# Optimization experiments

Hardware: AMD Instinct MI355X
Metric: run time of the kernel (lower is better)

The kernel has to match this reference:

```python
import jax, jax.numpy as jnp
import numpy as np

B, D, L = 8, 512, 4096
NHEAD = 8
HEAD_DIM = D // NHEAD
TRUNC_STD = 0.02


def setup_inputs() -> dict:
    key = jax.random.key(0)
    ks = jax.random.split(key, 7)
    return {
        "x": jax.random.normal(ks[0], (B, D, L, 1), jnp.float32),
        "y": jax.random.normal(ks[1], (B, D, 1, 1), jnp.float32),
        "Wq": jax.random.normal(ks[2], (D, D), jnp.float32) * TRUNC_STD,
        "Wk": jax.random.normal(ks[3], (D, D), jnp.float32) * TRUNC_STD,
        "Wv": jax.random.normal(ks[4], (D, D), jnp.float32) * TRUNC_STD,
        "WO_ring": jax.random.normal(ks[5], (D, D), jnp.float32) * TRUNC_STD,
        "bO_ring": jnp.zeros((D,), jnp.float32),
        "WO_star": jax.random.normal(ks[6], (D, D), jnp.float32) * TRUNC_STD,
        "bO_star": jnp.zeros((D,), jnp.float32),
    }


def reference(x, y, Wq, Wk, Wv, WO_ring, bO_ring, WO_star, bO_star):
    Bx, Dx, Lx, _ = x.shape
    hd = Dx // NHEAD
    scale = 1.0 / np.sqrt(hd).astype(np.float32)

    # concat relay token on the sequence axis, project q/k/v over channels
    xy = jnp.concatenate([x, y], axis=2)[..., 0]            # [B, D, L+1]
    xy = jnp.transpose(xy, (0, 2, 1))                       # [B, L+1, D]
    q = jnp.transpose(xy @ Wq, (0, 2, 1))                   # [B, D, L+1]
    k = jnp.transpose(xy @ Wk, (0, 2, 1))
    v = jnp.transpose(xy @ Wv, (0, 2, 1))

    # ---- ring (local window-3 + relay) attention over the L node tokens ----
    qn = q[:, :, :Lx].reshape(Bx, NHEAD, hd, Lx)            # [B,n,h,L]
    kn, vn = k[:, :, :Lx], v[:, :, :Lx]                     # [B,D,L]
    kr, vr = k[:, :, Lx], v[:, :, Lx]                       # [B,D]

    def window3(t):
        # extract_patches SAME with size 3: slot w holds t[:, :, l-1+w], zero-padded
        tp = jnp.pad(t, ((0, 0), (0, 0), (1, 1)))
        tw = jnp.stack([tp[:, :, w:w + Lx] for w in range(3)], axis=2)  # [B,D,3,L]
        return tw.reshape(Bx, NHEAD, hd, 3, Lx)

    kr_b = jnp.broadcast_to(kr.reshape(Bx, NHEAD, hd, 1, 1), (Bx, NHEAD, hd, 1, Lx))
    vr_b = jnp.broadcast_to(vr.reshape(Bx, NHEAD, hd, 1, 1), (Bx, NHEAD, hd, 1, Lx))
    kw = jnp.concatenate([window3(kn), kr_b], axis=3)       # [B,n,h,4,L]
    vw = jnp.concatenate([window3(vn), vr_b], axis=3)

    scores = jnp.einsum('bnhl,bnhwl->bnwl', qn, kw) * scale  # [B,n,4,L]
    alphas = jax.nn.softmax(scores, axis=2)                  # softmax over window
    att = jnp.einsum('bnwl,bnhwl->bnhl', alphas, vw).reshape(Bx, Dx, Lx)
    nodes = jnp.einsum('bdl,de->bel', att, WO_ring) + bO_ring[None, :, None]
    nodes = nodes[..., None]                                 # [B, D, L, 1]

    # ---- star (relay) attention: relay query attends to all L+1 tokens ----
    qr = q[:, :, Lx].reshape(Bx, NHEAD, 1, hd)              # [B,n,1,h]
    ka = k.reshape(Bx, NHEAD, hd, Lx + 1)                   # [B,n,h,L+1]
    va = v.reshape(Bx, NHEAD, hd, Lx + 1)
    s = jnp.einsum('bnoh,bnhl->bnol', qr, ka) * scale       # [B,n,1,L+1]
    a = jax.nn.softmax(s, axis=-1)
    att_r = jnp.einsum('bnol,bnhl->bnoh', a, va).reshape(Bx, Dx)
    relay = (att_r @ WO_star + bO_star).reshape(Bx, Dx, 1, 1)

    return nodes, relay
```

## Files before the change

kernel.cpp:

```cpp
#include <hip/hip_runtime.h>

#define BB 8
#define DD 512
#define LL 4096
#define NH 8
#define HD 64
#define SCALE 0.125f
#define NCH 16
#define CH 256

typedef __attribute__((ext_vector_type(8))) short short8;
typedef __attribute__((ext_vector_type(4))) float f32x4;

static __device__ __forceinline__ float bf2f(unsigned short u) {
  union { float f; unsigned int i; } c; c.i = ((unsigned int)u) << 16; return c.f;
}
static __device__ __forceinline__ unsigned short f2bf(float f) {
  union { float f; unsigned int i; } c; c.f = f;
  unsigned int i = c.i;
  unsigned int r = (i + 0x7fffu + ((i >> 16) & 1u)) >> 16;
  return (unsigned short)r;
}

static __device__ __forceinline__ void gload_lds16(const void* g, void* l) {
  __builtin_amdgcn_global_load_lds(
      (const __attribute__((address_space(1))) void*)g,
      (__attribute__((address_space(3))) void*)l, 16, 0, 0);
}

static __device__ __forceinline__ float waveSum(float v) {
#pragma unroll
  for (int o = 32; o; o >>= 1) v += __shfl_down(v, o, 64);
  return v;
}
static __device__ __forceinline__ float waveMax(float v) {
#pragma unroll
  for (int o = 32; o; o >>= 1) v = fmaxf(v, __shfl_down(v, o, 64));
  return v;
}
static __device__ __forceinline__ float grp8Sum(float v) {
  v += __shfl_xor(v, 1, 8);
  v += __shfl_xor(v, 2, 8);
  v += __shfl_xor(v, 4, 8);
  return v;
}
static __device__ float blockSum(float v, float* red) {
  const int lane = threadIdx.x & 63, wid = threadIdx.x >> 6;
  const int nw = (int)(blockDim.x >> 6);
  v = waveSum(v);
  if (lane == 0) red[wid] = v;
  __syncthreads();
  if (wid == 0) {
    float t = (lane < nw) ? red[lane] : 0.f;
    t = waveSum(t);
    if (lane == 0) red[0] = t;
  }
  __syncthreads();
  float r = red[0];
  __syncthreads();
  return r;
}
static __device__ float blockMax(float v, float* red) {
  const int lane = threadIdx.x & 63, wid = threadIdx.x >> 6;
  const int nw = (int)(blockDim.x >> 6);
  v = waveMax(v);
  if (lane == 0) red[wid] = v;
  __syncthreads();
  if (wid == 0) {
    float t = (lane < nw) ? red[lane] : -1e30f;
    t = waveMax(t);
    if (lane == 0) red[0] = t;
  }
  __syncthreads();
  float r = red[0];
  __syncthreads();
  return r;
}

__global__ __launch_bounds__(256) void prep_w4(
    const float* __restrict__ w0, const float* __restrict__ w1,
    const float* __restrict__ w2, const float* __restrict__ w3,
    unsigned short* __restrict__ o0, unsigned short* __restrict__ o1,
    unsigned short* __restrict__ o2, unsigned short* __restrict__ o3) {
  const int s = blockIdx.z;
  const float* win = (s == 0) ? w0 : (s == 1) ? w1 : (s == 2) ? w2 : w3;
  unsigned short* wout = (s == 0) ? o0 : (s == 1) ? o1 : (s == 2) ? o2 : o3;
  const int d0 = blockIdx.y * 64;
  const int m0 = blockIdx.x * 64;
  __shared__ float t[64][65];
  const int tid = threadIdx.x;
  const int r = tid >> 4;
  const int c4 = (tid & 15) * 4;
#pragma unroll
  for (int p = 0; p < 4; p++) {
    const float4 v = *(const float4*)(win + (size_t)(d0 + p * 16 + r) * DD + m0 + c4);
    *(float4*)&t[p * 16 + r][c4] = v;
  }
  __syncthreads();
#pragma unroll
  for (int p = 0; p < 4; p++) {
    const int ll = p * 16 + r;
    ushort4 o;
    o.x = f2bf(t[c4 + 0][ll]);
    o.y = f2bf(t[c4 + 1][ll]);
    o.z = f2bf(t[c4 + 2][ll]);
    o.w = f2bf(t[c4 + 3][ll]);
    *(ushort4*)(wout + (size_t)(m0 + ll) * DD + d0 + c4) = o;
  }
}

__global__ __launch_bounds__(256) void prep_x(
    const float* __restrict__ x, unsigned short* __restrict__ xt) {
  const int b = blockIdx.z;
  const int e0 = blockIdx.y * 64;
  const int l0 = blockIdx.x * 64;
  __shared__ float t[64][65];
  const int tid = threadIdx.x;
  const int r = tid >> 4;
  const int c4 = (tid & 15) * 4;
  const float* xb = x + (size_t)b * DD * LL;
#pragma unroll
  for (int p = 0; p < 4; p++) {
    const float4 v = *(const float4*)(xb + (size_t)(e0 + p * 16 + r) * LL + l0 + c4);
    *(float4*)&t[p * 16 + r][c4] = v;
  }
  __syncthreads();
#pragma unroll
  for (int p = 0; p < 4; p++) {
    const int ll = p * 16 + r;
    ushort4 o;
    o.x = f2bf(t[c4 + 0][ll]);
    o.y = f2bf(t[c4 + 1][ll]);
    o.z = f2bf(t[c4 + 2][ll]);
    o.w = f2bf(t[c4 + 3][ll]);
    *(ushort4*)(xt + ((size_t)b * LL + l0 + ll) * DD + e0 + c4) = o;
  }
}

#define STAGEH(g, s)                                       \
  do {                                                     \
    gload_lds16((g) + sgoff, (s) + sloff);                 \
    gload_lds16((g) + sgoff + 32, (s) + sloff + 4096);     \
  } while (0)

#define READ_A(dst, base, ib)                                           \
  _Pragma("unroll") for (int i = 0; i < 4; i++) {                       \
    dst[i][0] = *(const short8*)((base) + ((ib) + i) * 512);            \
    dst[i][1] = *(const short8*)((base) + ((ib) + i) * 512 + 4096);     \
  }

#define READ_B(base, qn_)                                               \
  _Pragma("unroll") for (int j = 0; j < 2; j++) {                       \
    bb[j][0] = *(const short8*)((base) + (qn_) * 1024 + j * 512);       \
    bb[j][1] = *(const short8*)((base) + (qn_) * 1024 + j * 512 + 4096);\
  }

#define MFMA16(AF, IO, JO)                                                    \
  __builtin_amdgcn_s_setprio(1);                                              \
  _Pragma("unroll") for (int i = 0; i < 4; i++)                               \
  _Pragma("unroll") for (int j = 0; j < 2; j++) {                             \
    acc[(IO) + i][(JO) + j] = __builtin_amdgcn_mfma_f32_16x16x32_bf16(        \
        AF[i][0], bb[j][0], acc[(IO) + i][(JO) + j], 0, 0, 0);                \
    acc[(IO) + i][(JO) + j] = __builtin_amdgcn_mfma_f32_16x16x32_bf16(        \
        AF[i][1], bb[j][1], acc[(IO) + i][(JO) + j], 0, 0, 0);                \
  }                                                                           \
  __builtin_amdgcn_s_setprio(0);

#define PHASE_SYNC_PRE                                     \
  __builtin_amdgcn_s_barrier();                            \
  asm volatile("s_waitcnt lgkmcnt(0)" ::: "memory");       \
  __builtin_amdgcn_sched_barrier(0);

#define PHASE_SYNC_POST                                    \
  __builtin_amdgcn_sched_barrier(0);                       \
  __builtin_amdgcn_s_barrier();

__global__ __launch_bounds__(512, 2) void qkv_mfma_8ph(
    const unsigned short* __restrict__ Wt, const unsigned short* __restrict__ Xt,
    unsigned short* __restrict__ qn, unsigned short* __restrict__ kn,
    unsigned short* __restrict__ vn) {
  extern __shared__ __align__(16) unsigned short sm[];
  const int wgid = blockIdx.x + 16 * (blockIdx.y + 6 * blockIdx.z);
  const int swz = (wgid & 7) * 96 + (wgid >> 3);
  const int b = swz / 96;
  const int rem = swz - b * 96;
  const int n0 = (rem / 6) * 256;
  const int m0 = (rem % 6) * 256;
  const int tid = threadIdx.x;
  const int lane = tid & 63, w = tid >> 6;
  const int wm = w >> 2, wn = w & 3;
  const int l15 = lane & 15, lh = lane >> 4;

  const unsigned short* Ag = Wt + (size_t)m0 * DD;
  const unsigned short* Bg = Xt + ((size_t)b * LL + n0) * DD;

  const int kswz = (lh << 3) ^ ((l15 & 8) << 1);
  const unsigned short* aB = sm + wm * 8192 + l15 * 32 + kswz;
  const unsigned short* bB = sm + 32768 + (wn >> 1) * 8192 + (wn & 1) * 2048 +
                             l15 * 32 + kswz;

  const int srow = (w << 4) + (lane >> 2);
  const size_t sgoff = (size_t)srow * DD + ((size_t)(((lane & 3) << 3) ^ ((srow & 8) << 1)));
  const int sloff = w * 512;

  f32x4 acc[8][4];
#pragma unroll
  for (int i = 0; i < 8; i++)
#pragma unroll
    for (int j = 0; j < 4; j++) acc[i][j] = (f32x4){0.f, 0.f, 0.f, 0.f};

  STAGEH(Ag, sm);
  STAGEH(Ag + 128 * DD, sm + 8192);
  STAGEH(Bg, sm + 32768);
  STAGEH(Bg + 128 * DD, sm + 32768 + 8192);
  STAGEH(Ag + 64, sm + 16384);
  STAGEH(Ag + 128 * DD + 64, sm + 16384 + 8192);
  asm volatile("s_waitcnt vmcnt(4)" ::: "memory");
  __builtin_amdgcn_s_barrier();

  short8 a0[4][2], a1[4][2], bb[2][2];
  for (int u = 0; u < 8; ++u) {
    const int slot = u & 1;
    const unsigned short* aS = aB + slot * 16384;
    const unsigned short* bS = bB + slot * 16384;
    const unsigned short* An = Ag + (u + 2) * 64;
    const unsigned short* Bn = Bg + (u + 1) * 64;
    unsigned short* sAd = sm + slot * 16384;
    unsigned short* sBd = sm + 32768 + (slot ^ 1) * 16384;

    READ_A(a0, aS, 0);
    READ_B(bS, 0);
    if (u < 7) STAGEH(Bn, sBd);
    PHASE_SYNC_PRE
    MFMA16(a0, 0, 0)
    PHASE_SYNC_POST
    READ_A(a1, aS, 4);
    if (u < 7) STAGEH(Bn + 128 * DD, sBd + 8192);
    PHASE_SYNC_PRE
    MFMA16(a1, 4, 0)
    PHASE_SYNC_POST
    READ_B(bS, 1);
    if (u < 6) STAGEH(An, sAd);
    PHASE_SYNC_PRE
    MFMA16(a0, 0, 2)
    PHASE_SYNC_POST
    if (u < 6) STAGEH(An + 128 * DD, sAd + 8192);
    __builtin_amdgcn_s_barrier();
    asm volatile("s_waitcnt lgkmcnt(0)" ::: "memory");
    __builtin_amdgcn_sched_barrier(0);
    MFMA16(a1, 4, 2)
    __builtin_amdgcn_sched_barrier(0);
    if (u < 6) {
      asm volatile("s_waitcnt vmcnt(4)" ::: "memory");
    } else if (u == 6) {
      asm volatile("s_waitcnt vmcnt(0)" ::: "memory");
    }
    __builtin_amdgcn_s_barrier();
  }

  __syncthreads();
#pragma unroll
  for (int i = 0; i < 8; i++)
#pragma unroll
    for (int j = 0; j < 4; j++) {
      const int dloc = wm * 128 + i * 16 + lh * 4;
      const int lloc = wn * 64 + j * 16 + l15;
      ushort4 pk;
      pk.x = f2bf(acc[i][j][0]);
      pk.y = f2bf(acc[i][j][1]);
      pk.z = f2bf(acc[i][j][2]);
      pk.w = f2bf(acc[i][j][3]);
      *(ushort4*)((char*)sm + ((lloc * 512 + dloc * 2) ^ ((lloc & 7) << 4))) = pk;
    }
  __syncthreads();
  const int sector = m0 >> 9;
  unsigned short* outp = ((sector == 0) ? qn : (sector == 1) ? kn : vn) +
                         (size_t)b * LL * DD + (m0 & 511);
#pragma unroll
  for (int it = 0; it < 16; it++) {
    const int flat = it * 8192 + tid * 16;
    const int lloc = flat >> 9;
    const int off = flat & 511;
    const short8 vdat =
        *(const short8*)((const char*)sm + lloc * 512 + (off ^ ((lloc & 7) << 4)));
    *(short8*)(outp + (size_t)(n0 + lloc) * DD + (off >> 1)) = vdat;
  }
}

__global__ __launch_bounds__(256) void nodes_mfma(
    const unsigned short* __restrict__ Wt, const unsigned short* __restrict__ At,
    const float* __restrict__ bo, float* __restrict__ out) {
  const int wgid = blockIdx.x + 32 * (blockIdx.y + 4 * blockIdx.z);
  const int swz = (wgid & 7) * 128 + (wgid >> 3);
  const int b = swz >> 7;
  const int rem = swz & 127;
  const int n0 = (rem >> 2) * 128;
  const int m0 = (rem & 3) * 128;
  __shared__ short As[128 * 32];
  __shared__ short Bs[128 * 32];
  const int tid = threadIdx.x;
  const int lane = tid & 63, w = tid >> 6;
  const int wm = w & 1, wn = w >> 1;

  const unsigned short* Ag = Wt + (size_t)m0 * DD;
  const unsigned short* Bg = At + ((size_t)b * LL + n0) * DD;
  const int srow = lane >> 2;
  const int scol = (lane & 3) * 8;

  f32x4 acc[4][4];
#pragma unroll
  for (int i = 0; i < 4; i++)
#pragma unroll
    for (int j = 0; j < 4; j++) acc[i][j] = (f32x4){0.f, 0.f, 0.f, 0.f};

  for (int k0 = 0; k0 < DD; k0 += 32) {
    __syncthreads();
#pragma unroll
    for (int p = 0; p < 2; p++) {
      const int c = w * 2 + p;
      gload_lds16(Ag + (size_t)(c * 16 + srow) * DD + k0 + scol, (short*)As + c * 16 * 32);
      gload_lds16(Bg + (size_t)(c * 16 + srow) * DD + k0 + scol, (short*)Bs + c * 16 * 32);
    }
    __syncthreads();
    short8 af[4], bfr[4];
#pragma unroll
    for (int i = 0; i < 4; i++)
      af[i] = *(const short8*)&As[(wm * 64 + i * 16 + (lane & 15)) * 32 + (lane >> 4) * 8];
#pragma unroll
    for (int j = 0; j < 4; j++)
      bfr[j] = *(const short8*)&Bs[(wn * 64 + j * 16 + (lane & 15)) * 32 + (lane >> 4) * 8];
#pragma unroll
    for (int i = 0; i < 4; i++)
#pragma unroll
      for (int j = 0; j < 4; j++)
        acc[i][j] = __builtin_amdgcn_mfma_f32_16x16x32_bf16(af[i], bfr[j], acc[i][j], 0, 0, 0);
  }

  float* outp = out + (size_t)b * DD * LL;
  const int ebase = m0 + wm * 64;
  const int col0 = n0 + wn * 64 + (lane & 15);
#pragma unroll
  for (int i = 0; i < 4; i++) {
    const int e0 = ebase + i * 16 + (lane >> 4) * 4;
#pragma unroll
    for (int j = 0; j < 4; j++) {
      const int cc = col0 + j * 16;
#pragma unroll
      for (int r = 0; r < 4; r++)
        outp[(size_t)(e0 + r) * LL + cc] = acc[i][j][r] + bo[e0 + r];
    }
  }
}

__global__ __launch_bounds__(256) void relay_qkv(
    const float* __restrict__ y, const float* __restrict__ Wq,
    const float* __restrict__ Wk, const float* __restrict__ Wv,
    float* __restrict__ qr, float* __restrict__ kr, float* __restrict__ vr) {
  const int b = blockIdx.y;
  const int d = blockIdx.x * 256 + threadIdx.x;
  __shared__ float ys[DD];
  for (int i = threadIdx.x; i < DD; i += 256) ys[i] = y[b * DD + i];
  __syncthreads();
  float aq = 0.f, ak = 0.f, av = 0.f;
  for (int e = 0; e < DD; e++) {
    const float yv = ys[e];
    aq = fmaf(yv, Wq[(size_t)e * DD + d], aq);
    ak = fmaf(yv, Wk[(size_t)e * DD + d], ak);
    av = fmaf(yv, Wv[(size_t)e * DD + d], av);
  }
  qr[b * DD + d] = aq;
  kr[b * DD + d] = ak;
  vr[b * DD + d] = av;
}

__global__ __launch_bounds__(256) void local_attn(
    const unsigned short* __restrict__ qn, const unsigned short* __restrict__ kn,
    const unsigned short* __restrict__ vn, const float* __restrict__ kr,
    const float* __restrict__ vr, unsigned short* __restrict__ att_t) {
  const int b = blockIdx.z, n = blockIdx.y;
  const int tid = threadIdx.x;
  const int li = tid >> 3, dl = tid & 7;
  const int l = blockIdx.x * 32 + li;
  __shared__ float krs[HD], vrs[HD];
  const int rb = b * DD + n * HD;
  if (tid < HD) { krs[tid] = kr[rb + tid]; vrs[tid] = vr[rb + tid]; }
  __syncthreads();

  const size_t rowbase = ((size_t)b * LL + l) * DD + n * HD + dl * 8;
  const unsigned short* qp = qn + rowbase;
  const unsigned short* kp = kn + rowbase;
  const unsigned short* vp = vn + rowbase;
  const bool has_m = (l > 0), has_p = (l < LL - 1);
  const long moff = has_m ? -(long)DD : 0;
  const long poff = has_p ? (long)DD : 0;

  const short8 q8 = *(const short8*)qp;
  const short8 km8 = *(const short8*)(kp + moff);
  const short8 k08 = *(const short8*)kp;
  const short8 kp8 = *(const short8*)(kp + poff);

  float s0 = 0.f, s1 = 0.f, s2 = 0.f, s3 = 0.f;
  float qf[8];
#pragma unroll
  for (int j = 0; j < 8; j++) {
    qf[j] = bf2f((unsigned short)q8[j]);
    s0 = fmaf(qf[j], bf2f((unsigned short)km8[j]), s0);
    s1 = fmaf(qf[j], bf2f((unsigned short)k08[j]), s1);
    s2 = fmaf(qf[j], bf2f((unsigned short)kp8[j]), s2);
    s3 = fmaf(qf[j], krs[dl * 8 + j], s3);
  }
  s0 = grp8Sum(s0) * SCALE;
  s1 = grp8Sum(s1) * SCALE;
  s2 = grp8Sum(s2) * SCALE;
  s3 = grp8Sum(s3) * SCALE;
  if (!has_m) s0 = 0.f;
  if (!has_p) s2 = 0.f;
  const float m = fmaxf(fmaxf(s0, s1), fmaxf(s2, s3));
  const float e0 = __expf(s0 - m), e1 = __expf(s1 - m);
  const float e2 = __expf(s2 - m), e3 = __expf(s3 - m);
  const float inv = 1.f / (e0 + e1 + e2 + e3);
  const float a0 = has_m ? e0 * inv : 0.f;
  const float a1 = e1 * inv;
  const float a2 = has_p ? e2 * inv : 0.f;
  const float a3 = e3 * inv;

  const short8 vm8 = *(const short8*)(vp + moff);
  const short8 v08 = *(const short8*)vp;
  const short8 vp8 = *(const short8*)(vp + poff);
  short8 o8;
#pragma unroll
  for (int j = 0; j < 8; j++) {
    float o = a0 * bf2f((unsigned short)vm8[j]) + a1 * bf2f((unsigned short)v08[j]) +
              a2 * bf2f((unsigned short)vp8[j]) + a3 * vrs[dl * 8 + j];
    o8[j] = (short)f2bf(o);
  }
  *(short8*)(att_t + rowbase) = o8;
}

__global__ __launch_bounds__(256) void relay_attn_part(
    const float* __restrict__ qr, const unsigned short* __restrict__ kn,
    const unsigned short* __restrict__ vn, float* __restrict__ part) {
  const int ch = blockIdx.x, n = blockIdx.y, b = blockIdx.z;
  const int tid = threadIdx.x;
  const int li = tid >> 3, dl = tid & 7;
  __shared__ float qs[HD];
  __shared__ float sv[CH];
  __shared__ float red[17];
  __shared__ float os[32][68];
  const int rb = b * DD + n * HD;
  if (tid < HD) qs[tid] = qr[rb + tid];
  __syncthreads();
  const size_t base = ((size_t)b * LL + ch * CH) * DD + n * HD + dl * 8;

#pragma unroll
  for (int it = 0; it < 8; it++) {
    const int lr2 = it * 32 + li;
    const short8 kc = *(const short8*)(kn + base + (size_t)lr2 * DD);
    float p = 0.f;
#pragma unroll
    for (int j = 0; j < 8; j++) p = fmaf(qs[dl * 8 + j], bf2f((unsigned short)kc[j]), p);
    p = grp8Sum(p);
    if (dl == 0) sv[lr2] = p * SCALE;
  }
  __syncthreads();
  const float s = sv[tid];
  const float m = blockMax(s, red);
  const float pp = __expf(s - m);
  sv[tid] = pp;
  const float sum = blockSum(pp, red);

  float oc[8];
#pragma unroll
  for (int j = 0; j < 8; j++) oc[j] = 0.f;
#pragma unroll
  for (int it = 0; it < 8; it++) {
    const int lr2 = it * 32 + li;
    const float p = sv[lr2];
    const short8 vc = *(const short8*)(vn + base + (size_t)lr2 * DD);
#pragma unroll
    for (int j = 0; j < 8; j++) oc[j] = fmaf(p, bf2f((unsigned short)vc[j]), oc[j]);
  }
#pragma unroll
  for (int j = 0; j < 8; j++) os[li][dl * 8 + j] = oc[j];
  __syncthreads();
  float* po = part + (((size_t)b * NH + n) * NCH + ch) * 68;
  if (tid < HD) {
    float t = 0.f;
#pragma unroll 8
    for (int g = 0; g < 32; g++) t += os[g][tid];
    po[tid] = t;
  }
  if (tid == 64) { po[64] = m; po[65] = sum; }
}

__global__ __launch_bounds__(64) void relay_attn_combine(
    const float* __restrict__ qr, const float* __restrict__ krr,
    const float* __restrict__ vrr, const float* __restrict__ part,
    float* __restrict__ attr) {
  const int n = blockIdx.x, b = blockIdx.y;
  const int h = threadIdx.x;
  const int rb = b * DD + n * HD;
  float t = qr[rb + h] * krr[rb + h];
  t = waveSum(t);
  const float s_r = __shfl(t, 0, 64) * SCALE;
  const float* po = part + (((size_t)b * NH + n) * NCH) * 68;
  float M = s_r;
#pragma unroll
  for (int c = 0; c < NCH; c++) M = fmaxf(M, po[c * 68 + 64]);
  float S = __expf(s_r - M);
  float o = S * vrr[rb + h];
#pragma unroll
  for (int c = 0; c < NCH; c++) {
    const float e = __expf(po[c * 68 + 64] - M);
    S = fmaf(po[c * 68 + 65], e, S);
    o = fmaf(po[c * 68 + h], e, o);
  }
  attr[rb + h] = o / S;
}

__global__ __launch_bounds__(256) void relay_proj(
    const float* __restrict__ attr, const float* __restrict__ Wstar,
    const float* __restrict__ bstar, float* __restrict__ out) {
  const int b = blockIdx.y;
  const int e = blockIdx.x * 256 + threadIdx.x;
  __shared__ float as[DD];
  for (int i = threadIdx.x; i < DD; i += 256) as[i] = attr[b * DD + i];
  __syncthreads();
  float acc = bstar[e];
  for (int d = 0; d < DD; d++) acc = fmaf(as[d], Wstar[(size_t)d * DD + e], acc);
  out[(size_t)BB * DD * LL + b * DD + e] = acc;
}

extern "C" void kernel_launch(void* const* d_in, const int* in_sizes, int n_in,
                              void* d_out, int out_size, void* d_ws, size_t ws_size,
                              hipStream_t stream) {
  const float* x   = (const float*)d_in[0];
  const float* y   = (const float*)d_in[1];
  const float* Wq  = (const float*)d_in[2];
  const float* Wk  = (const float*)d_in[3];
  const float* Wv  = (const float*)d_in[4];
  const float* WOr = (const float*)d_in[5];
  const float* bOr = (const float*)d_in[6];
  const float* WOs = (const float*)d_in[7];
  const float* bOs = (const float*)d_in[8];
  float* out = (float*)d_out;

  char* ws = (char*)d_ws;
  const size_t SZ = (size_t)BB * DD * LL * sizeof(unsigned short);
  unsigned short* qn  = (unsigned short*)(ws);
  unsigned short* kn  = (unsigned short*)(ws + SZ);
  unsigned short* vn  = (unsigned short*)(ws + 2 * SZ);
  unsigned short* xt  = (unsigned short*)(ws + 3 * SZ);
  unsigned short* att_t = xt;
  unsigned short* Wallt = (unsigned short*)(ws + 4 * SZ);
  unsigned short* WOrt  = (unsigned short*)(ws + 4 * SZ + 1536 * 512 * 2);
  float* qr   = (float*)(ws + 4 * SZ + 2048 * 512 * 2);
  float* kr   = qr + BB * DD;
  float* vr   = kr + BB * DD;
  float* attr = vr + BB * DD;
  float* part = attr + BB * DD;

  static int smaxset = 0;
  if (!smaxset) {
    (void)hipFuncSetAttribute((const void*)qkv_mfma_8ph,
                              hipFuncAttributeMaxDynamicSharedMemorySize, 131072);
    smaxset = 1;
  }

  prep_w4<<<dim3(8, 8, 4), 256, 0, stream>>>(
      Wq, Wk, Wv, WOr,
      Wallt, Wallt + (size_t)512 * 512, Wallt + (size_t)1024 * 512, WOrt);
  prep_x<<<dim3(64, 8, BB), 256, 0, stream>>>(x, xt);

  qkv_mfma_8ph<<<dim3(16, 6, BB), 512, 131072, stream>>>(Wallt, xt, qn, kn, vn);
  relay_qkv<<<dim3(DD / 256, BB), 256, 0, stream>>>(y, Wq, Wk, Wv, qr, kr, vr);
  local_attn<<<dim3(LL / 32, NH, BB), 256, 0, stream>>>(qn, kn, vn, kr, vr, att_t);
  nodes_mfma<<<dim3(32, 4, BB), 256, 0, stream>>>(WOrt, att_t, bOr, out);
  relay_attn_part<<<dim3(NCH, NH, BB), 256, 0, stream>>>(qr, kn, vn, part);
  relay_attn_combine<<<dim3(NH, BB), 64, 0, stream>>>(qr, kr, vr, part, attr);
  relay_proj<<<dim3(DD / 256, BB), 256, 0, stream>>>(attr, WOs, bOs, out);
}
```

Baseline: 310.6 us.

## Stage K/V window rows in LDS for local attention; drop QKV workgroup swizzle

```diff
diff --git a/kernel.cpp b/kernel.cpp
--- a/kernel.cpp
+++ b/kernel.cpp
@@ -180,12 +180,9 @@
     unsigned short* __restrict__ qn, unsigned short* __restrict__ kn,
     unsigned short* __restrict__ vn) {
   extern __shared__ __align__(16) unsigned short sm[];
-  const int wgid = blockIdx.x + 16 * (blockIdx.y + 6 * blockIdx.z);
-  const int swz = (wgid & 7) * 96 + (wgid >> 3);
-  const int b = swz / 96;
-  const int rem = swz - b * 96;
-  const int n0 = (rem / 6) * 256;
-  const int m0 = (rem % 6) * 256;
+  const int b = blockIdx.z;
+  const int m0 = blockIdx.y * 256;
+  const int n0 = blockIdx.x * 256;
   const int tid = threadIdx.x;
   const int lane = tid & 63, w = tid >> 6;
   const int wm = w >> 2, wn = w & 3;
@@ -380,24 +377,40 @@
   const int b = blockIdx.z, n = blockIdx.y;
   const int tid = threadIdx.x;
   const int li = tid >> 3, dl = tid & 7;
-  const int l = blockIdx.x * 32 + li;
+  const int l0 = blockIdx.x * 32;
+  const int l = l0 + li;
   __shared__ float krs[HD], vrs[HD];
+  __shared__ __align__(16) char ksb[34 * 128];
+  __shared__ __align__(16) char vsb[34 * 128];
   const int rb = b * DD + n * HD;
   if (tid < HD) { krs[tid] = kr[rb + tid]; vrs[tid] = vr[rb + tid]; }
+
+  {
+    const int s1 = tid >> 3;
+    const int gl1 = min(max(l0 - 1 + s1, 0), LL - 1);
+    const size_t gb1 = ((size_t)b * LL + gl1) * DD + n * HD + dl * 8;
+    const int so1 = s1 * 128 + dl * 16;
+    *(short8*)(ksb + so1) = *(const short8*)(kn + gb1);
+    *(short8*)(vsb + so1) = *(const short8*)(vn + gb1);
+    if (tid < 16) {
+      const int s2 = 32 + (tid >> 3);
+      const int gl2 = min(l0 - 1 + s2, LL - 1);
+      const size_t gb2 = ((size_t)b * LL + gl2) * DD + n * HD + dl * 8;
+      const int so2 = s2 * 128 + dl * 16;
+      *(short8*)(ksb + so2) = *(const short8*)(kn + gb2);
+      *(short8*)(vsb + so2) = *(const short8*)(vn + gb2);
+    }
+  }
   __syncthreads();
 
   const size_t rowbase = ((size_t)b * LL + l) * DD + n * HD + dl * 8;
-  const unsigned short* qp = qn + rowbase;
-  const unsigned short* kp = kn + rowbase;
-  const unsigned short* vp = vn + rowbase;
   const bool has_m = (l > 0), has_p = (l < LL - 1);
-  const long moff = has_m ? -(long)DD : 0;
-  const long poff = has_p ? (long)DD : 0;
-
-  const short8 q8 = *(const short8*)qp;
-  const short8 km8 = *(const short8*)(kp + moff);
-  const short8 k08 = *(const short8*)kp;
-  const short8 kp8 = *(const short8*)(kp + poff);
+  const int lo = dl * 16;
+
+  const short8 q8 = *(const short8*)(qn + rowbase);
+  const short8 km8 = *(const short8*)(ksb + (li + 0) * 128 + lo);
+  const short8 k08 = *(const short8*)(ksb + (li + 1) * 128 + lo);
+  const short8 kp8 = *(const short8*)(ksb + (li + 2) * 128 + lo);
 
   float s0 = 0.f, s1 = 0.f, s2 = 0.f, s3 = 0.f;
   float qf[8];
@@ -424,9 +437,9 @@
   const float a2 = has_p ? e2 * inv : 0.f;
   const float a3 = e3 * inv;
 
-  const short8 vm8 = *(const short8*)(vp + moff);
-  const short8 v08 = *(const short8*)vp;
-  const short8 vp8 = *(const short8*)(vp + poff);
+  const short8 vm8 = *(const short8*)(vsb + (li + 0) * 128 + lo);
+  const short8 v08 = *(const short8*)(vsb + (li + 1) * 128 + lo);
+  const short8 vp8 = *(const short8*)(vsb + (li + 2) * 128 + lo);
   short8 o8;
 #pragma unroll
   for (int j = 0; j < 8; j++) {
```

Measured after the change: 307.3 us. Within noise of the previous version (-1.1%).
